# Optimization experiments

Hardware: AMD Instinct MI355X
Metric: run time of the kernel (lower is better)

Reference implementation:

```python
import jax, jax.numpy as jnp
import numpy as np

B, L, D, H = 4, 1024, 768, 6
DH = D // H
EPS = 1e-5


def setup_inputs() -> dict:
    key = jax.random.key(0)
    kq, kk, kv, kl, kw = jax.random.split(key, 5)
    Q = jax.random.normal(kq, (B, L, D), jnp.float32)
    K = jax.random.normal(kk, (B, L, D), jnp.float32)
    V = jax.random.normal(kv, (B, L, D), jnp.float32)
    # realistic padding: each batch element has a valid length in [L//2, L]
    lengths = jax.random.randint(kl, (B,), L // 2, L + 1)
    valid = jnp.arange(L)[None, :] < lengths[:, None]          # (B, L)
    pad_mask = valid[:, :, None] & valid[:, None, :]           # (B, L, L), True = keep
    bx_packed = ~valid                                         # (B, L), True = padded
    # BatchNorm affine params (per-head channels)
    g1 = jnp.ones((H,), jnp.float32)
    b1 = jnp.zeros((H,), jnp.float32)
    g2 = jnp.ones((H,), jnp.float32)
    b2 = jnp.zeros((H,), jnp.float32)
    # posterior gate: Linear(H, 2)
    Wp = jax.random.normal(kw, (2, H), jnp.float32) * (1.0 / np.sqrt(H))
    bp = jnp.zeros((2,), jnp.float32)
    return {"Q": Q, "K": K, "V": V, "pad_mask": pad_mask, "bx_packed": bx_packed,
            "g1": g1, "b1": b1, "g2": g2, "b2": b2, "Wp": Wp, "bp": bp}


def _split_heads(x):
    b, l, _ = x.shape
    return x.reshape(b, l, H, DH).transpose(0, 2, 1, 3)  # (B, H, L, DH)


def _batchnorm(x, g, b):
    # x: (B, H, N); training-mode BatchNorm1d over channels H (stats over B and N)
    m = x.mean(axis=(0, 2), keepdims=True)
    v = x.var(axis=(0, 2), keepdims=True)  # biased, as torch uses for normalization
    return (x - m) * jax.lax.rsqrt(v + EPS) * g[None, :, None] + b[None, :, None]


def _remove_nan(x):
    return jnp.where(jnp.isnan(x), jnp.zeros_like(x), x)


def reference(Q, K, V, pad_mask, bx_packed, g1, b1, g2, b2, Wp, bp):
    Qh, Kh, Vh = _split_heads(Q), _split_heads(K), _split_heads(V)
    b, h, l, _ = Qh.shape
    # DistMatrix: negative squared Euclidean distance between query/key vectors
    # scores[b,h,i,j] = -||Q_i - K_j||^2, via the GEMM-friendly expansion
    q2 = jnp.sum(Qh * Qh, axis=-1)                     # (B, H, L)
    k2 = jnp.sum(Kh * Kh, axis=-1)                     # (B, H, L)
    qk = jnp.einsum("bhid,bhjd->bhij", Qh, Kh)         # (B, H, L, L)
    co = -(q2[..., :, None] + k2[..., None, :] - 2.0 * qk)
    # norm1 over flattened L*L
    co = _batchnorm(co.reshape(b, h, l * l), g1, b1).reshape(b, h, l, l)
    # zero out positions where pad_mask is False (in-place masked fill in torch)
    co = jnp.where(pad_mask[:, None, :, :], co, 0.0)
    co = jax.nn.softmax(co, axis=-1)
    co = _remove_nan(co)
    # column-sum attention mass per key position
    w = co.sum(axis=-2)                                # (B, H, L)
    w = _batchnorm(w, g2, b2).transpose(0, 2, 1)       # (B, L, H)
    # posterior gate: Linear(H,2) + softmax, take class-0 probability
    w = jax.nn.softmax(w @ Wp.T + bp, axis=-1)[..., 0]  # (B, L)
    w = _remove_nan(w)
    w = jnp.where(bx_packed, -jnp.inf, w)
    w = jax.nn.softmax(w, axis=-1)
    w = _remove_nan(w)[..., None]                      # (B, L, 1)
    return co, w, Vh
```

## Files before the change

kernel.cpp:

```cpp
#include <hip/hip_runtime.h>
#include <stdint.h>
#include <stddef.h>

#define BB 4
#define LL 1024
#define DD 768
#define HH 6
#define DHH 128
#define EPS 1e-5f

#define CO_ELEMS 25165824
#define W_ELEMS  4096

#define OFF_Q2 0
#define OFF_K2 24576
#define OFF_WC 49152
#define OFF_SP 73728
#define OFF_A1 79872
#define OFF_C1 79880

typedef __attribute__((ext_vector_type(8))) short short8;
typedef __attribute__((ext_vector_type(4))) float f32x4;

__device__ __forceinline__ short8 ld_bf8(const float* __restrict__ p) {
    const float4 a = *(const float4*)(p);
    const float4 b = *(const float4*)(p + 4);
    short8 r;
    r[0] = (short)(__float_as_uint(a.x) >> 16);
    r[1] = (short)(__float_as_uint(a.y) >> 16);
    r[2] = (short)(__float_as_uint(a.z) >> 16);
    r[3] = (short)(__float_as_uint(a.w) >> 16);
    r[4] = (short)(__float_as_uint(b.x) >> 16);
    r[5] = (short)(__float_as_uint(b.y) >> 16);
    r[6] = (short)(__float_as_uint(b.z) >> 16);
    r[7] = (short)(__float_as_uint(b.w) >> 16);
    return r;
}

__global__ void k_zero(float* __restrict__ wcol) {
    int g = blockIdx.x * 256 + threadIdx.x;
    if (g < 24576) wcol[g] = 0.0f;
}

__global__ void k_rownorm(const float* __restrict__ Q,
                          const float* __restrict__ K,
                          float* __restrict__ ws) {
    int gid = blockIdx.x * 256 + threadIdx.x;
    int sub = gid & 3;
    int rg  = gid >> 2;
    int which = (rg >= 24576);
    int rid = which ? rg - 24576 : rg;
    int bh = rid >> 10, i = rid & 1023;
    int b = bh / HH, h = bh - b * HH;
    const float* src = (which ? K : Q) + (size_t)(b * LL + i) * DD + h * DHH;
    float s = 0.f;
#pragma unroll
    for (int kk = 0; kk < 8; kk++) {
        float4 v = *(const float4*)(src + (sub + 4 * kk) * 4);
        s += v.x * v.x + v.y * v.y + v.z * v.z + v.w * v.w;
    }
    s += __shfl_xor(s, 1);
    s += __shfl_xor(s, 2);
    if (sub == 0) ws[(which ? OFF_K2 : OFF_Q2) + rid] = s;
}

__global__ void k_vh(const float* __restrict__ V, float* __restrict__ out) {
    int cid = blockIdx.x * 256 + threadIdx.x;
    if (cid >= 786432) return;
    int d4 = cid & 31;
    int rest = cid >> 5;
    int l = rest & 1023;
    int bh = rest >> 10;
    int b = bh / HH, h = bh - b * HH;
    float4 v = *(const float4*)(V + (size_t)(b * LL + l) * DD + h * DHH + d4 * 4);
    *(float4*)(out + (size_t)cid * 4) = v;
}

__device__ __forceinline__ void gemm_qk(const float* __restrict__ Qb,
                                        const float* __restrict__ Kb,
                                        int ibase, int jbase, int lm, int quad,
                                        f32x4 acc[2][4]) {
#pragma unroll
    for (int kk = 0; kk < 4; kk++) {
        const int d0 = kk * 32 + quad * 8;
        short8 af[2], bfr[4];
        af[0] = ld_bf8(Qb + (size_t)(ibase + lm) * DD + d0);
        af[1] = ld_bf8(Qb + (size_t)(ibase + 16 + lm) * DD + d0);
#pragma unroll
        for (int tj = 0; tj < 4; tj++)
            bfr[tj] = ld_bf8(Kb + (size_t)(jbase + tj * 16 + lm) * DD + d0);
#pragma unroll
        for (int ti = 0; ti < 2; ti++)
#pragma unroll
            for (int tj = 0; tj < 4; tj++)
                acc[ti][tj] = __builtin_amdgcn_mfma_f32_16x16x32_bf16(af[ti], bfr[tj], acc[ti][tj], 0, 0, 0);
    }
}

__global__ __launch_bounds__(256) void k_gemm_S(
        const float* __restrict__ Q, const float* __restrict__ Km,
        const float* __restrict__ q2, const float* __restrict__ k2,
        float* __restrict__ co, float* __restrict__ statsP) {
    const int bh = blockIdx.z, b = bh / HH, h = bh - b * HH;
    const int tid = threadIdx.x, lane = tid & 63, wave = tid >> 6;
    const int wr = wave >> 1, wc = wave & 1;
    const int ibase = blockIdx.y * 64 + wr * 32;
    const int jbase = blockIdx.x * 128 + wc * 64;
    const int lm = lane & 15, quad = lane >> 4;
    const float* Qb = Q + (size_t)b * LL * DD + h * DHH;
    const float* Kb = Km + (size_t)b * LL * DD + h * DHH;

    f32x4 acc[2][4];
#pragma unroll
    for (int ti = 0; ti < 2; ti++)
#pragma unroll
        for (int tj = 0; tj < 4; tj++) acc[ti][tj] = (f32x4)(0.0f);
    gemm_qk(Qb, Kb, ibase, jbase, lm, quad, acc);

    float q2v[2][4], k2v[4];
#pragma unroll
    for (int ti = 0; ti < 2; ti++)
#pragma unroll
        for (int r = 0; r < 4; r++)
            q2v[ti][r] = q2[bh * 1024 + ibase + ti * 16 + quad * 4 + r];
#pragma unroll
    for (int tj = 0; tj < 4; tj++)
        k2v[tj] = k2[bh * 1024 + jbase + tj * 16 + lm];

    float s = 0.f, s2 = 0.f;
#pragma unroll
    for (int ti = 0; ti < 2; ti++)
#pragma unroll
        for (int tj = 0; tj < 4; tj++)
#pragma unroll
            for (int r = 0; r < 4; r++) {
                int i = ibase + ti * 16 + quad * 4 + r;
                int j = jbase + tj * 16 + lm;
                float S = 2.0f * acc[ti][tj][r] - q2v[ti][r] - k2v[tj];
                co[(size_t)(bh * 1024 + i) * 1024 + j] = S;
                s += S; s2 += S * S;
            }

    __shared__ float rA[256], rB[256];
    rA[tid] = s; rB[tid] = s2;
    __syncthreads();
    for (int off = 128; off > 0; off >>= 1) {
        if (tid < off) { rA[tid] += rA[tid + off]; rB[tid] += rB[tid + off]; }
        __syncthreads();
    }
    if (tid == 0) {
        int blk = blockIdx.y * 8 + blockIdx.x;
        int base = (bh * 128 + blk) * 2;
        statsP[base] = rA[0];
        statsP[base + 1] = rB[0];
    }
}

__global__ void k_stats(const float* __restrict__ statsP,
                        const float* __restrict__ g1, const float* __restrict__ b1,
                        float* __restrict__ a1, float* __restrict__ c1) {
    __shared__ float rA[256], rB[256];
    const int t = threadIdx.x;
    for (int h = 0; h < HH; h++) {
        float s = 0.f, s2 = 0.f;
        for (int m = t; m < 512; m += 256) {
            int b = m >> 7, blk = m & 127;
            int base = ((b * HH + h) * 128 + blk) * 2;
            s += statsP[base]; s2 += statsP[base + 1];
        }
        rA[t] = s; rB[t] = s2;
        __syncthreads();
        for (int off = 128; off > 0; off >>= 1) {
            if (t < off) { rA[t] += rA[t + off]; rB[t] += rB[t + off]; }
            __syncthreads();
        }
        if (t == 0) {
            const float N = 4194304.f;
            float m_ = rA[0] / N;
            float var = fmaxf(rB[0] / N - m_ * m_, 0.0f);
            float r = rsqrtf(var + EPS);
            float a = r * g1[h];
            a1[h] = a;
            c1[h] = b1[h] - m_ * a;
        }
        __syncthreads();
    }
}

__global__ __launch_bounds__(256) void k_normexp(
        float* __restrict__ co,
        const float* __restrict__ a1, const float* __restrict__ c1,
        const unsigned char* __restrict__ bx, float* __restrict__ wcol) {
    const int bh = blockIdx.y;
    const int b = bh / HH, h = bh - b * HH;
    const int strip = blockIdx.x;
    const int t = threadIdx.x;
    float* base = co + ((size_t)bh << 20) + ((size_t)strip << 14);
    const float a = a1[h], c = c1[h];

    const unsigned char* bxb = bx + b * LL;
    const uchar4 m4 = *(const uchar4*)(bxb + t * 4);
    const bool vj0 = (m4.x == 0), vj1 = (m4.y == 0), vj2 = (m4.z == 0), vj3 = (m4.w == 0);

    float4 buf[16];
    float rp[16];
#pragma unroll
    for (int r = 0; r < 16; r++) {
        const int i = strip * 16 + r;
        const bool vi = (bxb[i] == 0);
        float4 s4 = *(const float4*)(base + r * 1024 + t * 4);
        float4 e;
        e.x = (vi && vj0) ? __expf(fminf(a * s4.x + c, 60.0f)) : 1.0f;
        e.y = (vi && vj1) ? __expf(fminf(a * s4.y + c, 60.0f)) : 1.0f;
        e.z = (vi && vj2) ? __expf(fminf(a * s4.z + c, 60.0f)) : 1.0f;
        e.w = (vi && vj3) ? __expf(fminf(a * s4.w + c, 60.0f)) : 1.0f;
        buf[r] = e;
        rp[r] = e.x + e.y + e.z + e.w;
    }

    __shared__ float pr[16][257];
    __shared__ float pr2[16][17];
    __shared__ float inv[16];
#pragma unroll
    for (int r = 0; r < 16; r++) pr[r][t] = rp[r];
    __syncthreads();
    {
        int r = t >> 4, k = t & 15;
        float s = 0.f;
#pragma unroll
        for (int j = 0; j < 16; j++) s += pr[r][k * 16 + j];
        pr2[r][k] = s;
    }
    __syncthreads();
    if (t < 16) {
        float s = 0.f;
#pragma unroll
        for (int k = 0; k < 16; k++) s += pr2[t][k];
        inv[t] = 1.0f / s;
    }
    __syncthreads();

    float cs0 = 0.f, cs1 = 0.f, cs2 = 0.f, cs3 = 0.f;
#pragma unroll
    for (int r = 0; r < 16; r++) {
        const float iv = inv[r];
        float4 v = buf[r];
        v.x *= iv; v.y *= iv; v.z *= iv; v.w *= iv;
        *(float4*)(base + r * 1024 + t * 4) = v;
        cs0 += v.x; cs1 += v.y; cs2 += v.z; cs3 += v.w;
    }
    float* wc = wcol + bh * 1024 + t * 4;
    atomicAdd(wc + 0, cs0);
    atomicAdd(wc + 1, cs1);
    atomicAdd(wc + 2, cs2);
    atomicAdd(wc + 3, cs3);
}

__global__ __launch_bounds__(1024) void k_tail(
        const float* __restrict__ wcol, const unsigned char* __restrict__ bx,
        const float* __restrict__ g2, const float* __restrict__ b2,
        const float* __restrict__ Wp, const float* __restrict__ bp,
        float* __restrict__ wout) {
    __shared__ float red[1024];
    __shared__ float red2[1024];
    __shared__ float a2s[HH], c2s[HH];
    __shared__ float xbuf[4096];
    const int t = threadIdx.x;

    for (int h = 0; h < HH; h++) {
        float s = 0.f, s2 = 0.f;
#pragma unroll
        for (int p = 0; p < 4; p++) {
            int idx = t + p * 1024;
            int b = idx >> 10, l = idx & 1023;
            float v = wcol[(size_t)(b * HH + h) * 1024 + l];
            s += v; s2 += v * v;
        }
        red[t] = s; red2[t] = s2;
        __syncthreads();
        for (int off = 512; off > 0; off >>= 1) {
            if (t < off) { red[t] += red[t + off]; red2[t] += red2[t + off]; }
            __syncthreads();
        }
        if (t == 0) {
            const float N = 4096.f;
            float m = red[0] / N;
            float var = fmaxf(red2[0] / N - m * m, 0.0f);
            float r = rsqrtf(var + EPS);
            float a = r * g2[h];
            a2s[h] = a;
            c2s[h] = b2[h] - m * a;
        }
        __syncthreads();
    }

    const float bp0 = bp[0], bp1 = bp[1];
#pragma unroll
    for (int p = 0; p < 4; p++) {
        int idx = t + p * 1024;
        int b = idx >> 10, l = idx & 1023;
        float z0 = bp0, z1 = bp1;
#pragma unroll
        for (int h = 0; h < HH; h++) {
            float wn = a2s[h] * wcol[(size_t)(b * HH + h) * 1024 + l] + c2s[h];
            z0 += wn * Wp[h];
            z1 += wn * Wp[HH + h];
        }
        float pc = 1.0f / (1.0f + __expf(z1 - z0));
        xbuf[idx] = bx[b * LL + l] ? -INFINITY : pc;
    }
    __syncthreads();

    for (int b = 0; b < BB; b++) {
        float x = xbuf[b * 1024 + t];
        red[t] = x;
        __syncthreads();
        for (int off = 512; off > 0; off >>= 1) {
            if (t < off) red[t] = fmaxf(red[t], red[t + off]);
            __syncthreads();
        }
        float mx = red[0];
        __syncthreads();
        float e = __expf(x - mx);
        red[t] = e;
        __syncthreads();
        for (int off = 512; off > 0; off >>= 1) {
            if (t < off) red[t] += red[t + off];
            __syncthreads();
        }
        float sum = red[0];
        __syncthreads();
        wout[b * 1024 + t] = e / sum;
    }
}

extern "C" void kernel_launch(void* const* d_in, const int* in_sizes, int n_in,
                              void* d_out, int out_size, void* d_ws, size_t ws_size,
                              hipStream_t stream) {
    const float* Q  = (const float*)d_in[0];
    const float* K  = (const float*)d_in[1];
    const float* V  = (const float*)d_in[2];
    const unsigned char* bx = (const unsigned char*)d_in[4];
    const float* g1 = (const float*)d_in[5];
    const float* b1 = (const float*)d_in[6];
    const float* g2 = (const float*)d_in[7];
    const float* b2 = (const float*)d_in[8];
    const float* Wp = (const float*)d_in[9];
    const float* bp = (const float*)d_in[10];

    float* out  = (float*)d_out;
    float* co   = out;
    float* wout = out + CO_ELEMS;
    float* vh   = out + CO_ELEMS + W_ELEMS;

    float* ws = (float*)d_ws;
    float* q2     = ws + OFF_Q2;
    float* k2     = ws + OFF_K2;
    float* wcol   = ws + OFF_WC;
    float* statsP = ws + OFF_SP;
    float* a1     = ws + OFF_A1;
    float* c1     = ws + OFF_C1;

    k_zero<<<96, 256, 0, stream>>>(wcol);
    k_rownorm<<<768, 256, 0, stream>>>(Q, K, ws);
    k_vh<<<3072, 256, 0, stream>>>(V, vh);
    k_gemm_S<<<dim3(8, 16, BB * HH), 256, 0, stream>>>(Q, K, q2, k2, co, statsP);
    k_stats<<<1, 256, 0, stream>>>(statsP, g1, b1, a1, c1);
    k_normexp<<<dim3(64, 24), 256, 0, stream>>>(co, a1, c1, bx, wcol);
    k_tail<<<1, 1024, 0, stream>>>(wcol, bx, g2, b2, Wp, bp, wout);
}
```

Measured before the change: 305.2 us.

## Replace column-sum atomics with partial buffer reduction and use nontemporal stores

Drops the zeroing kernel and the per-block atomicAdds into the column-sum buffer. Each normexp block now writes its partial column sums to a per-strip buffer, and a new reduce kernel sums those partials and also computes the second BatchNorm's statistics. The large co and Vh outputs are written with nontemporal stores to avoid cache pollution. The tail kernel is rewritten to use wave shuffles instead of long shared-memory tree reductions. The cost is an extra launch and extra partial-sum traffic.

Measured after the change: 274.6 us. 10.0% less time.

```diff
diff --git a/kernel.cpp b/kernel.cpp
--- a/kernel.cpp
+++ b/kernel.cpp
@@ -12,12 +12,13 @@
 #define CO_ELEMS 25165824
 #define W_ELEMS  4096
 
-#define OFF_Q2 0
-#define OFF_K2 24576
-#define OFF_WC 49152
-#define OFF_SP 73728
-#define OFF_A1 79872
-#define OFF_C1 79880
+#define OFF_Q2  0
+#define OFF_K2  24576
+#define OFF_WC  49152
+#define OFF_SP  73728
+#define OFF_AC  79872
+#define OFF_SS  79888
+#define OFF_WP  81920
 
 typedef __attribute__((ext_vector_type(8))) short short8;
 typedef __attribute__((ext_vector_type(4))) float f32x4;
@@ -37,11 +38,6 @@
     return r;
 }
 
-__global__ void k_zero(float* __restrict__ wcol) {
-    int g = blockIdx.x * 256 + threadIdx.x;
-    if (g < 24576) wcol[g] = 0.0f;
-}
-
 __global__ void k_rownorm(const float* __restrict__ Q,
                           const float* __restrict__ K,
                           float* __restrict__ ws) {
@@ -72,29 +68,8 @@
     int l = rest & 1023;
     int bh = rest >> 10;
     int b = bh / HH, h = bh - b * HH;
-    float4 v = *(const float4*)(V + (size_t)(b * LL + l) * DD + h * DHH + d4 * 4);
-    *(float4*)(out + (size_t)cid * 4) = v;
-}
-
-__device__ __forceinline__ void gemm_qk(const float* __restrict__ Qb,
-                                        const float* __restrict__ Kb,
-                                        int ibase, int jbase, int lm, int quad,
-                                        f32x4 acc[2][4]) {
-#pragma unroll
-    for (int kk = 0; kk < 4; kk++) {
-        const int d0 = kk * 32 + quad * 8;
-        short8 af[2], bfr[4];
-        af[0] = ld_bf8(Qb + (size_t)(ibase + lm) * DD + d0);
-        af[1] = ld_bf8(Qb + (size_t)(ibase + 16 + lm) * DD + d0);
-#pragma unroll
-        for (int tj = 0; tj < 4; tj++)
-            bfr[tj] = ld_bf8(Kb + (size_t)(jbase + tj * 16 + lm) * DD + d0);
-#pragma unroll
-        for (int ti = 0; ti < 2; ti++)
-#pragma unroll
-            for (int tj = 0; tj < 4; tj++)
-                acc[ti][tj] = __builtin_amdgcn_mfma_f32_16x16x32_bf16(af[ti], bfr[tj], acc[ti][tj], 0, 0, 0);
-    }
+    f32x4 v = *(const f32x4*)(V + (size_t)(b * LL + l) * DD + h * DHH + d4 * 4);
+    __builtin_nontemporal_store(v, (f32x4*)(out + (size_t)cid * 4));
 }
 
 __global__ __launch_bounds__(256) void k_gemm_S(
@@ -115,7 +90,22 @@
     for (int ti = 0; ti < 2; ti++)
 #pragma unroll
         for (int tj = 0; tj < 4; tj++) acc[ti][tj] = (f32x4)(0.0f);
-    gemm_qk(Qb, Kb, ibase, jbase, lm, quad, acc);
+
+#pragma unroll
+    for (int kk = 0; kk < 4; kk++) {
+        const int d0 = kk * 32 + quad * 8;
+        short8 af[2], bfr[4];
+        af[0] = ld_bf8(Qb + (size_t)(ibase + lm) * DD + d0);
+        af[1] = ld_bf8(Qb + (size_t)(ibase + 16 + lm) * DD + d0);
+#pragma unroll
+        for (int tj = 0; tj < 4; tj++)
+            bfr[tj] = ld_bf8(Kb + (size_t)(jbase + tj * 16 + lm) * DD + d0);
+#pragma unroll
+        for (int ti = 0; ti < 2; ti++)
+#pragma unroll
+            for (int tj = 0; tj < 4; tj++)
+                acc[ti][tj] = __builtin_amdgcn_mfma_f32_16x16x32_bf16(af[ti], bfr[tj], acc[ti][tj], 0, 0, 0);
+    }
 
     float q2v[2][4], k2v[4];
 #pragma unroll
@@ -158,7 +148,7 @@
 
 __global__ void k_stats(const float* __restrict__ statsP,
                         const float* __restrict__ g1, const float* __restrict__ b1,
-                        float* __restrict__ a1, float* __restrict__ c1) {
+                        float* __restrict__ ac) {
     __shared__ float rA[256], rB[256];
     const int t = threadIdx.x;
     for (int h = 0; h < HH; h++) {
@@ -180,42 +170,41 @@
             float var = fmaxf(rB[0] / N - m_ * m_, 0.0f);
             float r = rsqrtf(var + EPS);
             float a = r * g1[h];
-            a1[h] = a;
-            c1[h] = b1[h] - m_ * a;
+            ac[h] = a;
+            ac[8 + h] = b1[h] - m_ * a;
         }
         __syncthreads();
     }
 }
 
 __global__ __launch_bounds__(256) void k_normexp(
-        float* __restrict__ co,
-        const float* __restrict__ a1, const float* __restrict__ c1,
-        const unsigned char* __restrict__ bx, float* __restrict__ wcol) {
+        float* __restrict__ co, const float* __restrict__ ac,
+        const unsigned char* __restrict__ bx, float* __restrict__ wcolP) {
     const int bh = blockIdx.y;
     const int b = bh / HH, h = bh - b * HH;
     const int strip = blockIdx.x;
     const int t = threadIdx.x;
     float* base = co + ((size_t)bh << 20) + ((size_t)strip << 14);
-    const float a = a1[h], c = c1[h];
+    const float a = ac[h], c = ac[8 + h];
 
     const unsigned char* bxb = bx + b * LL;
     const uchar4 m4 = *(const uchar4*)(bxb + t * 4);
     const bool vj0 = (m4.x == 0), vj1 = (m4.y == 0), vj2 = (m4.z == 0), vj3 = (m4.w == 0);
 
-    float4 buf[16];
+    f32x4 buf[16];
     float rp[16];
 #pragma unroll
     for (int r = 0; r < 16; r++) {
         const int i = strip * 16 + r;
         const bool vi = (bxb[i] == 0);
-        float4 s4 = *(const float4*)(base + r * 1024 + t * 4);
-        float4 e;
-        e.x = (vi && vj0) ? __expf(fminf(a * s4.x + c, 60.0f)) : 1.0f;
-        e.y = (vi && vj1) ? __expf(fminf(a * s4.y + c, 60.0f)) : 1.0f;
-        e.z = (vi && vj2) ? __expf(fminf(a * s4.z + c, 60.0f)) : 1.0f;
-        e.w = (vi && vj3) ? __expf(fminf(a * s4.w + c, 60.0f)) : 1.0f;
+        f32x4 s4 = *(const f32x4*)(base + r * 1024 + t * 4);
+        f32x4 e;
+        e[0] = (vi && vj0) ? __expf(fminf(a * s4[0] + c, 60.0f)) : 1.0f;
+        e[1] = (vi && vj1) ? __expf(fminf(a * s4[1] + c, 60.0f)) : 1.0f;
+        e[2] = (vi && vj2) ? __expf(fminf(a * s4[2] + c, 60.0f)) : 1.0f;
+        e[3] = (vi && vj3) ? __expf(fminf(a * s4[3] + c, 60.0f)) : 1.0f;
         buf[r] = e;
-        rp[r] = e.x + e.y + e.z + e.w;
+        rp[r] = e[0] + e[1] + e[2] + e[3];
     }
 
     __shared__ float pr[16][257];
@@ -244,55 +233,66 @@
 #pragma unroll
     for (int r = 0; r < 16; r++) {
         const float iv = inv[r];
-        float4 v = buf[r];
-        v.x *= iv; v.y *= iv; v.z *= iv; v.w *= iv;
-        *(float4*)(base + r * 1024 + t * 4) = v;
-        cs0 += v.x; cs1 += v.y; cs2 += v.z; cs3 += v.w;
-    }
-    float* wc = wcol + bh * 1024 + t * 4;
-    atomicAdd(wc + 0, cs0);
-    atomicAdd(wc + 1, cs1);
-    atomicAdd(wc + 2, cs2);
-    atomicAdd(wc + 3, cs3);
+        f32x4 v = buf[r];
+        v[0] *= iv; v[1] *= iv; v[2] *= iv; v[3] *= iv;
+        __builtin_nontemporal_store(v, (f32x4*)(base + r * 1024 + t * 4));
+        cs0 += v[0]; cs1 += v[1]; cs2 += v[2]; cs3 += v[3];
+    }
+    float4 wv; wv.x = cs0; wv.y = cs1; wv.z = cs2; wv.w = cs3;
+    *(float4*)&wcolP[((size_t)strip * 24 + bh) * 1024 + t * 4] = wv;
+}
+
+__global__ void k_wcol_reduce(const float* __restrict__ wcolP,
+                              float* __restrict__ wcol, float* __restrict__ ws2) {
+    const int t = threadIdx.x;
+    int g = blockIdx.x * 256 + t;
+    float s = 0.f;
+#pragma unroll 8
+    for (int strip = 0; strip < 64; strip++)
+        s += wcolP[(size_t)strip * 24576 + g];
+    wcol[g] = s;
+    float a = s, b = s * s;
+#pragma unroll
+    for (int off = 1; off < 64; off <<= 1) { a += __shfl_xor(a, off); b += __shfl_xor(b, off); }
+    __shared__ float sc[4][2];
+    if ((t & 63) == 0) { sc[t >> 6][0] = a; sc[t >> 6][1] = b; }
+    __syncthreads();
+    if (t == 0) {
+        ws2[blockIdx.x * 2]     = sc[0][0] + sc[1][0] + sc[2][0] + sc[3][0];
+        ws2[blockIdx.x * 2 + 1] = sc[0][1] + sc[1][1] + sc[2][1] + sc[3][1];
+    }
 }
 
 __global__ __launch_bounds__(1024) void k_tail(
-        const float* __restrict__ wcol, const unsigned char* __restrict__ bx,
+        const float* __restrict__ wcol, const float* __restrict__ ws2,
+        const unsigned char* __restrict__ bx,
         const float* __restrict__ g2, const float* __restrict__ b2,
         const float* __restrict__ Wp, const float* __restrict__ bp,
         float* __restrict__ wout) {
-    __shared__ float red[1024];
-    __shared__ float red2[1024];
-    __shared__ float a2s[HH], c2s[HH];
-    __shared__ float xbuf[4096];
-    const int t = threadIdx.x;
-
-    for (int h = 0; h < HH; h++) {
+    const int t = threadIdx.x, lane = t & 63, wv = t >> 6;
+    __shared__ float abuf[12];
+    __shared__ float xb[4096];
+    __shared__ float wred[16][2];
+
+    if (t < HH) {
         float s = 0.f, s2 = 0.f;
-#pragma unroll
-        for (int p = 0; p < 4; p++) {
-            int idx = t + p * 1024;
-            int b = idx >> 10, l = idx & 1023;
-            float v = wcol[(size_t)(b * HH + h) * 1024 + l];
-            s += v; s2 += v * v;
-        }
-        red[t] = s; red2[t] = s2;
-        __syncthreads();
-        for (int off = 512; off > 0; off >>= 1) {
-            if (t < off) { red[t] += red[t + off]; red2[t] += red2[t + off]; }
-            __syncthreads();
-        }
-        if (t == 0) {
-            const float N = 4096.f;
-            float m = red[0] / N;
-            float var = fmaxf(red2[0] / N - m * m, 0.0f);
-            float r = rsqrtf(var + EPS);
-            float a = r * g2[h];
-            a2s[h] = a;
-            c2s[h] = b2[h] - m * a;
-        }
-        __syncthreads();
-    }
+        for (int b = 0; b < 4; b++) {
+            int bh = b * HH + t;
+#pragma unroll
+            for (int sub = 0; sub < 4; sub++) {
+                int blk = bh * 4 + sub;
+                s += ws2[blk * 2];
+                s2 += ws2[blk * 2 + 1];
+            }
+        }
+        float m = s / 4096.f;
+        float var = fmaxf(s2 / 4096.f - m * m, 0.0f);
+        float r = rsqrtf(var + EPS);
+        float a = r * g2[t];
+        abuf[t] = a;
+        abuf[6 + t] = b2[t] - m * a;
+    }
+    __syncthreads();
 
     const float bp0 = bp[0], bp1 = bp[1];
 #pragma unroll
@@ -302,36 +302,35 @@
         float z0 = bp0, z1 = bp1;
 #pragma unroll
         for (int h = 0; h < HH; h++) {
-            float wn = a2s[h] * wcol[(size_t)(b * HH + h) * 1024 + l] + c2s[h];
+            float wn = abuf[h] * wcol[(size_t)(b * HH + h) * 1024 + l] + abuf[6 + h];
             z0 += wn * Wp[h];
             z1 += wn * Wp[HH + h];
         }
         float pc = 1.0f / (1.0f + __expf(z1 - z0));
-        xbuf[idx] = bx[b * LL + l] ? -INFINITY : pc;
-    }
-    __syncthreads();
-
-    for (int b = 0; b < BB; b++) {
-        float x = xbuf[b * 1024 + t];
-        red[t] = x;
-        __syncthreads();
-        for (int off = 512; off > 0; off >>= 1) {
-            if (t < off) red[t] = fmaxf(red[t], red[t + off]);
-            __syncthreads();
-        }
-        float mx = red[0];
-        __syncthreads();
-        float e = __expf(x - mx);
-        red[t] = e;
-        __syncthreads();
-        for (int off = 512; off > 0; off >>= 1) {
-            if (t < off) red[t] += red[t + off];
-            __syncthreads();
-        }
-        float sum = red[0];
-        __syncthreads();
-        wout[b * 1024 + t] = e / sum;
-    }
+        xb[idx] = bx[b * LL + l] ? -INFINITY : pc;
+    }
+    __syncthreads();
+
+    const int bb = t >> 8, tb = t & 255;
+    float4 xv = *(const float4*)&xb[bb * 1024 + tb * 4];
+    float mx = fmaxf(fmaxf(xv.x, xv.y), fmaxf(xv.z, xv.w));
+#pragma unroll
+    for (int off = 1; off < 64; off <<= 1) mx = fmaxf(mx, __shfl_xor(mx, off));
+    if (lane == 0) wred[wv][0] = mx;
+    __syncthreads();
+    mx = fmaxf(fmaxf(wred[bb * 4][0], wred[bb * 4 + 1][0]),
+               fmaxf(wred[bb * 4 + 2][0], wred[bb * 4 + 3][0]));
+    float e0 = __expf(xv.x - mx), e1 = __expf(xv.y - mx);
+    float e2 = __expf(xv.z - mx), e3 = __expf(xv.w - mx);
+    float ss = e0 + e1 + e2 + e3;
+#pragma unroll
+    for (int off = 1; off < 64; off <<= 1) ss += __shfl_xor(ss, off);
+    if (lane == 0) wred[wv][1] = ss;
+    __syncthreads();
+    float sum = wred[bb * 4][1] + wred[bb * 4 + 1][1] + wred[bb * 4 + 2][1] + wred[bb * 4 + 3][1];
+    float4 o;
+    o.x = e0 / sum; o.y = e1 / sum; o.z = e2 / sum; o.w = e3 / sum;
+    *(float4*)&wout[bb * 1024 + tb * 4] = o;
 }
 
 extern "C" void kernel_launch(void* const* d_in, const int* in_sizes, int n_in,
@@ -358,14 +357,15 @@
     float* k2     = ws + OFF_K2;
     float* wcol   = ws + OFF_WC;
     float* statsP = ws + OFF_SP;
-    float* a1     = ws + OFF_A1;
-    float* c1     = ws + OFF_C1;
-
-    k_zero<<<96, 256, 0, stream>>>(wcol);
+    float* ac     = ws + OFF_AC;
+    float* ws2    = ws + OFF_SS;
+    float* wcolP  = ws + OFF_WP;
+
     k_rownorm<<<768, 256, 0, stream>>>(Q, K, ws);
     k_vh<<<3072, 256, 0, stream>>>(V, vh);
     k_gemm_S<<<dim3(8, 16, BB * HH), 256, 0, stream>>>(Q, K, q2, k2, co, statsP);
-    k_stats<<<1, 256, 0, stream>>>(statsP, g1, b1, a1, c1);
-    k_normexp<<<dim3(64, 24), 256, 0, stream>>>(co, a1, c1, bx, wcol);
-    k_tail<<<1, 1024, 0, stream>>>(wcol, bx, g2, b2, Wp, bp, wout);
-}
+    k_stats<<<1, 256, 0, stream>>>(statsP, g1, b1, ac);
+    k_normexp<<<dim3(64, 24), 256, 0, stream>>>(co, ac, bx, wcolP);
+    k_wcol_reduce<<<96, 256, 0, stream>>>(wcolP, wcol, ws2);
+    k_tail<<<1, 1024, 0, stream>>>(wcol, ws2, bx, g2, b2, Wp, bp, wout);
+}
```
